# Kernel optimization log

Measured on AMD Instinct MI355X. Metric: run time of the kernel, lower is better.

Reference implementation:

```python
import jax, jax.numpy as jnp
import numpy as np

HEADS = 16
D_MODEL = 1024
D_K = D_MODEL // HEADS


def setup_inputs() -> dict:
    key = jax.random.key(0)
    ks = jax.random.split(key, 11)
    B, S = 4, 2048
    scale = 1.0 / np.sqrt(D_MODEL)
    inp = {
        "query": jax.random.normal(ks[0], (B, S, D_MODEL), dtype=jnp.float32),
        "key": jax.random.normal(ks[1], (B, S, D_MODEL), dtype=jnp.float32),
        "value": jax.random.normal(ks[2], (B, S, D_MODEL), dtype=jnp.float32),
        "Wq": jax.random.normal(ks[3], (D_MODEL, D_MODEL), dtype=jnp.float32) * scale,
        "bq": jnp.zeros((D_MODEL,), dtype=jnp.float32),
        "Wk": jax.random.normal(ks[4], (D_MODEL, D_MODEL), dtype=jnp.float32) * scale,
        "bk": jnp.zeros((D_MODEL,), dtype=jnp.float32),
        "Wv": jax.random.normal(ks[5], (D_MODEL, D_MODEL), dtype=jnp.float32) * scale,
        "bv": jnp.zeros((D_MODEL,), dtype=jnp.float32),
        "Wo": jax.random.normal(ks[6], (D_MODEL, D_MODEL), dtype=jnp.float32) * scale,
        "bo": jnp.zeros((D_MODEL,), dtype=jnp.float32),
    }
    return inp


def reference(query, key, value, Wq, bq, Wk, bk, Wv, bv, Wo, bo):
    B, S, _ = query.shape
    # Linear projections, split into heads: [B,S,D] -> [B,H,S,d_k]
    def proj(x, W, b):
        y = x @ W.T + b
        return y.reshape(B, S, HEADS, D_K).transpose(0, 2, 1, 3)

    q = proj(query, Wq, bq)
    k = proj(key, Wk, bk)
    v = proj(value, Wv, bv)

    scores = jnp.einsum("bhqd,bhkd->bhqk", q, k) / jnp.sqrt(jnp.float32(D_K))
    p_attn = jax.nn.softmax(scores, axis=-1)  # dropout is identity in eval
    x = jnp.einsum("bhqk,bhkd->bhqd", p_attn, v)
    x = x.transpose(0, 2, 1, 3).reshape(B, S, HEADS * D_K)
    return x @ Wo.T + bo
```

## Files before the change

kernel.cpp:

```cpp
#include <hip/hip_runtime.h>
#include <hip/hip_bf16.h>
#include <stdint.h>

#define D_MODEL 1024
#define HEADS   16
#define DK      64
#define BATCH   4
#define SEQ     2048
#define MROWS   (BATCH * SEQ)

typedef __attribute__((ext_vector_type(8))) short bf16x8;
typedef __attribute__((ext_vector_type(4))) float f32x4;
typedef __attribute__((ext_vector_type(4))) unsigned int u32x4;
typedef __attribute__((ext_vector_type(2))) unsigned int u32x2;

__device__ __forceinline__ unsigned pk2bf(float a, float b) {
  __hip_bfloat162 h = __float22bfloat162_rn(float2{a, b});
  union { __hip_bfloat162 h; unsigned u; } c; c.h = h;
  return c.u;
}
__device__ __forceinline__ unsigned short n2bf(float f) {
  __hip_bfloat16 h = __float2bfloat16(f);
  union { __hip_bfloat16 h; unsigned short s; } c; c.h = h;
  return c.s;
}

__device__ __forceinline__ void gl_lds16(const void* g, void* l) {
  __builtin_amdgcn_global_load_lds(
      (const __attribute__((address_space(1))) unsigned int*)g,
      (__attribute__((address_space(3))) unsigned int*)l, 16, 0, 0);
}

__device__ __forceinline__ int swz64(int row, int col) {
  return row * 64 + (col ^ ((row & 7) << 3));
}

__global__ __launch_bounds__(256) void cvt4(const float* __restrict__ w0, const float* __restrict__ w1,
                                            const float* __restrict__ w2, const float* __restrict__ w3,
                                            unsigned short* __restrict__ o0, unsigned short* __restrict__ o1,
                                            unsigned short* __restrict__ o2, unsigned short* __restrict__ o3) {
  const int which = blockIdx.x >> 10;
  const float* in; unsigned short* out;
  if (which == 0)      { in = w0; out = o0; }
  else if (which == 1) { in = w1; out = o1; }
  else if (which == 2) { in = w2; out = o2; }
  else                 { in = w3; out = o3; }
  const int i = ((blockIdx.x & 1023) * 256 + threadIdx.x) * 4;
  f32x4 v = *(const f32x4*)(in + i);
  u32x2 w;
  w[0] = pk2bf(v[0], v[1]);
  w[1] = pk2bf(v[2], v[3]);
  *(u32x2*)(out + i) = w;
}

__global__ __launch_bounds__(256) void qkv_gemm(const float* __restrict__ Aq, const float* __restrict__ Ak,
                                                const float* __restrict__ Av,
                                                const unsigned short* __restrict__ Bq,
                                                const unsigned short* __restrict__ Bk,
                                                const unsigned short* __restrict__ Bv,
                                                const float* __restrict__ bq_, const float* __restrict__ bk_,
                                                const float* __restrict__ bv_,
                                                unsigned short* __restrict__ Qo, unsigned short* __restrict__ Ko,
                                                unsigned short* __restrict__ Vo) {
  __shared__ unsigned short As[128 * 40];
  __shared__ unsigned short Bs[128 * 32];

  const int which = blockIdx.x >> 9;
  const int bx = blockIdx.x & 511;
  const float* Af = which == 0 ? Aq : which == 1 ? Ak : Av;
  const unsigned short* Bw = which == 0 ? Bq : which == 1 ? Bk : Bv;
  const float* bias = which == 0 ? bq_ : which == 1 ? bk_ : bv_;

  const int tid = threadIdx.x;
  const int lane = tid & 63, wid = tid >> 6;
  const int l16 = lane & 15, lg = lane >> 4;
  const int wrow = (wid >> 1) * 64, wcol = (wid & 1) * 64;

  const int swzb = (bx & 7) * 64 + (bx >> 3);
  const int m0 = (swzb >> 3) * 128, n0 = (swzb & 7) * 128;

  f32x4 acc[4][4];
  const f32x4 zero = {0.f, 0.f, 0.f, 0.f};
#pragma unroll
  for (int i = 0; i < 4; ++i)
#pragma unroll
    for (int j = 0; j < 4; ++j) acc[i][j] = zero;

#pragma unroll 1
  for (int kt = 0; kt < D_MODEL / 32; ++kt) {
    const int k0 = kt * 32;
    __syncthreads();
    {
      const int ar = tid >> 1, ah = (tid & 1) * 16;
      const float* src = Af + (size_t)(m0 + ar) * D_MODEL + k0 + ah;
      f32x4 v0 = *(const f32x4*)src;
      f32x4 v1 = *(const f32x4*)(src + 4);
      f32x4 v2 = *(const f32x4*)(src + 8);
      f32x4 v3 = *(const f32x4*)(src + 12);
      u32x4 pa, pb;
      pa[0] = pk2bf(v0[0], v0[1]);
      pa[1] = pk2bf(v0[2], v0[3]);
      pa[2] = pk2bf(v1[0], v1[1]);
      pa[3] = pk2bf(v1[2], v1[3]);
      pb[0] = pk2bf(v2[0], v2[1]);
      pb[1] = pk2bf(v2[2], v2[3]);
      pb[2] = pk2bf(v3[0], v3[1]);
      pb[3] = pk2bf(v3[2], v3[3]);
      *(u32x4*)&As[ar * 40 + ah] = pa;
      *(u32x4*)&As[ar * 40 + ah + 8] = pb;
    }
    {
      const unsigned short* srcb = Bw + (size_t)n0 * D_MODEL + k0;
#pragma unroll
      for (int p = 0; p < 2; ++p) {
        const int e = wid * 512 + p * 2048 + lane * 8;
        gl_lds16(srcb + (size_t)(e >> 5) * D_MODEL + (e & 31),
                 (char*)Bs + wid * 1024 + p * 4096);
      }
    }
    __syncthreads();

    bf16x8 af[4], bfr[4];
#pragma unroll
    for (int i = 0; i < 4; ++i) {
      af[i]  = *(const bf16x8*)&As[(wrow + i * 16 + l16) * 40 + lg * 8];
      bfr[i] = *(const bf16x8*)&Bs[(wcol + i * 16 + l16) * 32 + lg * 8];
    }
#pragma unroll
    for (int i = 0; i < 4; ++i)
#pragma unroll
      for (int j = 0; j < 4; ++j)
        acc[i][j] = __builtin_amdgcn_mfma_f32_16x16x32_bf16(af[i], bfr[j], acc[i][j], 0, 0, 0);
  }

#pragma unroll
  for (int j = 0; j < 4; ++j) {
    const int col = n0 + wcol + j * 16 + l16;
    const float bv = bias[col];
    if (which == 2) {
      const int hh = col >> 6, dd = col & 63;
#pragma unroll
      for (int i = 0; i < 4; ++i) {
        const int row0 = m0 + wrow + i * 16 + lg * 4;
        u32x2 pw;
        pw[0] = pk2bf(acc[i][j][0] + bv, acc[i][j][1] + bv);
        pw[1] = pk2bf(acc[i][j][2] + bv, acc[i][j][3] + bv);
        unsigned short* dst = Vo +
            ((((size_t)(row0 >> 11) * HEADS + hh) * DK + dd) * SEQ + (row0 & (SEQ - 1)));
        *(u32x2*)dst = pw;
      }
    } else {
      unsigned short* Outp = which == 0 ? Qo : Ko;
#pragma unroll
      for (int i = 0; i < 4; ++i) {
        const int row0 = m0 + wrow + i * 16 + lg * 4;
#pragma unroll
        for (int r = 0; r < 4; ++r)
          Outp[(size_t)(row0 + r) * D_MODEL + col] = n2bf(acc[i][j][r] + bv);
      }
    }
  }
}

__global__ __launch_bounds__(256) void out_gemm(const unsigned short* __restrict__ Ab,
                                                const unsigned short* __restrict__ Bw,
                                                const float* __restrict__ bias,
                                                float* __restrict__ Outp) {
  __shared__ unsigned short As[128 * 32];
  __shared__ unsigned short Bs[128 * 32];

  const int tid = threadIdx.x;
  const int lane = tid & 63, wid = tid >> 6;
  const int l16 = lane & 15, lg = lane >> 4;
  const int wrow = (wid >> 1) * 64, wcol = (wid & 1) * 64;

  const int bx = blockIdx.x;
  const int swzb = (bx & 7) * 64 + (bx >> 3);
  const int m0 = (swzb >> 3) * 128, n0 = (swzb & 7) * 128;

  f32x4 acc[4][4];
  const f32x4 zero = {0.f, 0.f, 0.f, 0.f};
#pragma unroll
  for (int i = 0; i < 4; ++i)
#pragma unroll
    for (int j = 0; j < 4; ++j) acc[i][j] = zero;

#pragma unroll 1
  for (int kt = 0; kt < D_MODEL / 32; ++kt) {
    const int k0 = kt * 32;
    __syncthreads();
    {
      const unsigned short* srcb = Ab + (size_t)m0 * D_MODEL + k0;
#pragma unroll
      for (int p = 0; p < 2; ++p) {
        const int e = wid * 512 + p * 2048 + lane * 8;
        gl_lds16(srcb + (size_t)(e >> 5) * D_MODEL + (e & 31),
                 (char*)As + wid * 1024 + p * 4096);
      }
    }
    {
      const unsigned short* srcb = Bw + (size_t)n0 * D_MODEL + k0;
#pragma unroll
      for (int p = 0; p < 2; ++p) {
        const int e = wid * 512 + p * 2048 + lane * 8;
        gl_lds16(srcb + (size_t)(e >> 5) * D_MODEL + (e & 31),
                 (char*)Bs + wid * 1024 + p * 4096);
      }
    }
    __syncthreads();

    bf16x8 af[4], bfr[4];
#pragma unroll
    for (int i = 0; i < 4; ++i) {
      af[i]  = *(const bf16x8*)&As[(wrow + i * 16 + l16) * 32 + lg * 8];
      bfr[i] = *(const bf16x8*)&Bs[(wcol + i * 16 + l16) * 32 + lg * 8];
    }
#pragma unroll
    for (int i = 0; i < 4; ++i)
#pragma unroll
      for (int j = 0; j < 4; ++j)
        acc[i][j] = __builtin_amdgcn_mfma_f32_16x16x32_bf16(af[i], bfr[j], acc[i][j], 0, 0, 0);
  }

#pragma unroll
  for (int j = 0; j < 4; ++j) {
    const int col = n0 + wcol + j * 16 + l16;
    const float bv = bias[col];
#pragma unroll
    for (int i = 0; i < 4; ++i) {
      const int row0 = m0 + wrow + i * 16 + lg * 4;
#pragma unroll
      for (int r = 0; r < 4; ++r)
        Outp[(size_t)(row0 + r) * D_MODEL + col] = acc[i][j][r] + bv;
    }
  }
}

__global__ __launch_bounds__(256, 2) void attn_v9(const unsigned short* __restrict__ Qb,
                                                  const unsigned short* __restrict__ Kb,
                                                  const unsigned short* __restrict__ Vtg,
                                                  unsigned short* __restrict__ Xo) {
  __shared__ unsigned short Ks[2][64 * 64];
  __shared__ unsigned short Vt[2][64 * 64];
  __shared__ unsigned short Ps[4][64 * 64];

  const int tid = threadIdx.x;
  const int lane = tid & 63, w = tid >> 6;
  const int l16 = lane & 15, lg = lane >> 4;

  const int p = blockIdx.x;
  const int lb = (p & 7) * 64 + (p >> 3);
  const int qb = lb & 7, bh = lb >> 3;
  const int b = bh >> 4, h = bh & 15;

  const size_t srow0 = (size_t)b * SEQ + qb * 256;
  const unsigned short* Qp = Qb + srow0 * D_MODEL + h * DK;
  const unsigned short* Kp = Kb + (size_t)b * SEQ * D_MODEL + h * DK;
  const unsigned short* Vp = Vtg + (size_t)bh * DK * SEQ;

  const int sr = tid >> 2;
  const int scol = (tid & 3) * 16;

  bf16x8 qfrag[4][2];
#pragma unroll
  for (int qf = 0; qf < 4; ++qf)
#pragma unroll
    for (int kh = 0; kh < 2; ++kh)
      qfrag[qf][kh] = *(const bf16x8*)(Qp + (size_t)(w * 64 + qf * 16 + l16) * D_MODEL + kh * 32 + lg * 8);

  u32x4 kr0, kr1, vr0, vr1;
  {
    const unsigned short* ksrc = Kp + (size_t)sr * D_MODEL + scol;
    kr0 = *(const u32x4*)ksrc; kr1 = *(const u32x4*)(ksrc + 8);
    const unsigned short* vsrc = Vp + (size_t)sr * SEQ + scol;
    vr0 = *(const u32x4*)vsrc; vr1 = *(const u32x4*)(vsrc + 8);
  }

  float lsum[4];
  f32x4 acco[4][4];
  const f32x4 zero = {0.f, 0.f, 0.f, 0.f};
#pragma unroll
  for (int qf = 0; qf < 4; ++qf) {
    lsum[qf] = 0.f;
#pragma unroll
    for (int df = 0; df < 4; ++df) acco[qf][df] = zero;
  }

  const float SC = 0.125f * 1.4426950408889634f;
  unsigned short* Psw = Ps[w];
  const int srcbase = (lane & 48) | ((lane & 48) >> 2);

#pragma unroll 1
  for (int kb = 0; kb < SEQ / 64; ++kb) {
    const int buf = kb & 1;
    *(u32x4*)&Ks[buf][swz64(sr, scol)] = kr0;
    *(u32x4*)&Ks[buf][swz64(sr, scol + 8)] = kr1;
    *(u32x4*)&Vt[buf][swz64(sr, scol)] = vr0;
    *(u32x4*)&Vt[buf][swz64(sr, scol + 8)] = vr1;
    __syncthreads();
    if (kb + 1 < SEQ / 64) {
      const unsigned short* ksrc = Kp + (size_t)((kb + 1) * 64 + sr) * D_MODEL + scol;
      kr0 = *(const u32x4*)ksrc; kr1 = *(const u32x4*)(ksrc + 8);
      const unsigned short* vsrc = Vp + (size_t)sr * SEQ + (kb + 1) * 64 + scol;
      vr0 = *(const u32x4*)vsrc; vr1 = *(const u32x4*)(vsrc + 8);
    }

    f32x4 sc[4][4];
#pragma unroll
    for (int qf = 0; qf < 4; ++qf)
#pragma unroll
      for (int tf = 0; tf < 4; ++tf) sc[qf][tf] = zero;
#pragma unroll
    for (int tf = 0; tf < 4; ++tf) {
      bf16x8 k0 = *(const bf16x8*)&Ks[buf][swz64(tf * 16 + l16, lg * 8)];
      bf16x8 k1 = *(const bf16x8*)&Ks[buf][swz64(tf * 16 + l16, 32 + lg * 8)];
#pragma unroll
      for (int qf = 0; qf < 4; ++qf) {
        sc[qf][tf] = __builtin_amdgcn_mfma_f32_16x16x32_bf16(k0, qfrag[qf][0], sc[qf][tf], 0, 0, 0);
        sc[qf][tf] = __builtin_amdgcn_mfma_f32_16x16x32_bf16(k1, qfrag[qf][1], sc[qf][tf], 0, 0, 0);
      }
    }

#pragma unroll
    for (int qf = 0; qf < 4; ++qf) {
      float sum = 0.f;
#pragma unroll
      for (int tf = 0; tf < 4; ++tf)
#pragma unroll
        for (int r = 0; r < 4; ++r) {
          const float pv = __builtin_amdgcn_exp2f(sc[qf][tf][r] * SC);
          sc[qf][tf][r] = pv;
          sum += pv;
        }
      lsum[qf] += sum;
#pragma unroll
      for (int tf = 0; tf < 4; ++tf) {
        u32x2 pw;
        pw[0] = pk2bf(sc[qf][tf][0], sc[qf][tf][1]);
        pw[1] = pk2bf(sc[qf][tf][2], sc[qf][tf][3]);
        *(u32x2*)&Psw[swz64(qf * 16 + l16, tf * 16 + lg * 4)] = pw;
      }
    }

    bf16x8 pf[4][2];
#pragma unroll
    for (int qf = 0; qf < 4; ++qf)
#pragma unroll
      for (int k2 = 0; k2 < 2; ++k2)
        pf[qf][k2] = *(const bf16x8*)&Psw[swz64(qf * 16 + l16, k2 * 32 + lg * 8)];

#pragma unroll
    for (int df = 0; df < 4; ++df) {
      bf16x8 v0 = *(const bf16x8*)&Vt[buf][swz64(df * 16 + l16, lg * 8)];
      bf16x8 v1 = *(const bf16x8*)&Vt[buf][swz64(df * 16 + l16, 32 + lg * 8)];
#pragma unroll
      for (int qf = 0; qf < 4; ++qf) {
        acco[qf][df] = __builtin_amdgcn_mfma_f32_16x16x32_bf16(pf[qf][0], v0, acco[qf][df], 0, 0, 0);
        acco[qf][df] = __builtin_amdgcn_mfma_f32_16x16x32_bf16(pf[qf][1], v1, acco[qf][df], 0, 0, 0);
      }
    }
  }

#pragma unroll
  for (int qf = 0; qf < 4; ++qf) {
    lsum[qf] += __shfl_xor(lsum[qf], 16);
    lsum[qf] += __shfl_xor(lsum[qf], 32);
  }

  unsigned short* dst = Xo + (srow0 + w * 64) * D_MODEL + h * DK;
#pragma unroll
  for (int qf = 0; qf < 4; ++qf) {
    const float inv = 1.f / lsum[qf];
#pragma unroll
    for (int r = 0; r < 4; ++r) {
      const float rr = __shfl(inv, srcbase + r);
      const int row = qf * 16 + lg * 4 + r;
#pragma unroll
      for (int df = 0; df < 4; ++df)
        dst[(size_t)row * D_MODEL + df * 16 + l16] = n2bf(acco[qf][df][r] * rr);
    }
  }
}

extern "C" void kernel_launch(void* const* d_in, const int* in_sizes, int n_in,
                              void* d_out, int out_size, void* d_ws, size_t ws_size,
                              hipStream_t stream) {
  const float* query = (const float*)d_in[0];
  const float* key_  = (const float*)d_in[1];
  const float* value = (const float*)d_in[2];
  const float* Wq = (const float*)d_in[3];
  const float* bq = (const float*)d_in[4];
  const float* Wk = (const float*)d_in[5];
  const float* bk = (const float*)d_in[6];
  const float* Wv = (const float*)d_in[7];
  const float* bv = (const float*)d_in[8];
  const float* Wo = (const float*)d_in[9];
  const float* bo = (const float*)d_in[10];

  unsigned short* ws  = (unsigned short*)d_ws;
  unsigned short* WqB = ws;
  unsigned short* WkB = WqB + (1u << 20);
  unsigned short* WvB = WkB + (1u << 20);
  unsigned short* WoB = WvB + (1u << 20);
  unsigned short* Qb  = WoB + (1u << 20);
  unsigned short* Kb  = Qb + (size_t)MROWS * D_MODEL;
  unsigned short* Vtg = Kb + (size_t)MROWS * D_MODEL;
  unsigned short* Xb  = Vtg + (size_t)MROWS * D_MODEL;
  if (ws_size < (size_t)(4u * (1u << 20) + 4u * (size_t)MROWS * D_MODEL) * 2u) return;

  cvt4<<<4096, 256, 0, stream>>>(Wq, Wk, Wv, Wo, WqB, WkB, WvB, WoB);

  qkv_gemm<<<1536, 256, 0, stream>>>(query, key_, value, WqB, WkB, WvB, bq, bk, bv, Qb, Kb, Vtg);

  attn_v9<<<512, 256, 0, stream>>>(Qb, Kb, Vtg, Xb);

  out_gemm<<<512, 256, 0, stream>>>(Xb, WoB, bo, (float*)d_out);
}
```

Before: 241.0 us.

## Double-buffer GEMM LDS tiles with register prefetch and fold softmax scale into Q

Both projection GEMMs switch from a single LDS buffer filled by direct global-to-LDS loads to two LDS buffers filled from registers. The next K-tile is loaded into registers while the current tile is consumed, so each iteration needs one barrier instead of two and global latency is hidden behind MFMA work. Separately, the softmax scale (1/sqrt(dk)·log2e) is applied to Q in the QKV epilogue, which removes one multiply per score in the attention kernel. The cost is more LDS and register pressure, and the scaled Q is rounded to bf16 after scaling, which changes rounding slightly.

```diff
diff --git a/kernel.cpp b/kernel.cpp
--- a/kernel.cpp
+++ b/kernel.cpp
@@ -14,6 +14,8 @@
 typedef __attribute__((ext_vector_type(4))) unsigned int u32x4;
 typedef __attribute__((ext_vector_type(2))) unsigned int u32x2;
 
+#define SCQ 0.18033688011112042f
+
 __device__ __forceinline__ unsigned pk2bf(float a, float b) {
   __hip_bfloat162 h = __float22bfloat162_rn(float2{a, b});
   union { __hip_bfloat162 h; unsigned u; } c; c.h = h;
@@ -23,12 +25,6 @@
   __hip_bfloat16 h = __float2bfloat16(f);
   union { __hip_bfloat16 h; unsigned short s; } c; c.h = h;
   return c.s;
-}
-
-__device__ __forceinline__ void gl_lds16(const void* g, void* l) {
-  __builtin_amdgcn_global_load_lds(
-      (const __attribute__((address_space(1))) unsigned int*)g,
-      (__attribute__((address_space(3))) unsigned int*)l, 16, 0, 0);
 }
 
 __device__ __forceinline__ int swz64(int row, int col) {
@@ -62,8 +58,8 @@
                                                 const float* __restrict__ bv_,
                                                 unsigned short* __restrict__ Qo, unsigned short* __restrict__ Ko,
                                                 unsigned short* __restrict__ Vo) {
-  __shared__ unsigned short As[128 * 40];
-  __shared__ unsigned short Bs[128 * 32];
+  __shared__ unsigned short As[2][128 * 40];
+  __shared__ unsigned short Bs[2][128 * 32];
 
   const int which = blockIdx.x >> 9;
   const int bx = blockIdx.x & 511;
@@ -79,6 +75,10 @@
   const int swzb = (bx & 7) * 64 + (bx >> 3);
   const int m0 = (swzb >> 3) * 128, n0 = (swzb & 7) * 128;
 
+  const int sr2 = tid >> 1, sc16 = (tid & 1) * 16;
+  const float* aSrc = Af + (size_t)(m0 + sr2) * D_MODEL + sc16;
+  const unsigned short* bSrc = Bw + (size_t)(n0 + sr2) * D_MODEL + sc16;
+
   f32x4 acc[4][4];
   const f32x4 zero = {0.f, 0.f, 0.f, 0.f};
 #pragma unroll
@@ -86,45 +86,36 @@
 #pragma unroll
     for (int j = 0; j < 4; ++j) acc[i][j] = zero;
 
+  f32x4 a0 = *(const f32x4*)aSrc, a1 = *(const f32x4*)(aSrc + 4),
+        a2 = *(const f32x4*)(aSrc + 8), a3 = *(const f32x4*)(aSrc + 12);
+  u32x4 br0 = *(const u32x4*)bSrc, br1 = *(const u32x4*)(bSrc + 8);
+
 #pragma unroll 1
   for (int kt = 0; kt < D_MODEL / 32; ++kt) {
-    const int k0 = kt * 32;
+    const int buf = kt & 1;
+    u32x4 pa, pb;
+    pa[0] = pk2bf(a0[0], a0[1]); pa[1] = pk2bf(a0[2], a0[3]);
+    pa[2] = pk2bf(a1[0], a1[1]); pa[3] = pk2bf(a1[2], a1[3]);
+    pb[0] = pk2bf(a2[0], a2[1]); pb[1] = pk2bf(a2[2], a2[3]);
+    pb[2] = pk2bf(a3[0], a3[1]); pb[3] = pk2bf(a3[2], a3[3]);
+    *(u32x4*)&As[buf][sr2 * 40 + sc16] = pa;
+    *(u32x4*)&As[buf][sr2 * 40 + sc16 + 8] = pb;
+    *(u32x4*)&Bs[buf][sr2 * 32 + sc16] = br0;
+    *(u32x4*)&Bs[buf][sr2 * 32 + sc16 + 8] = br1;
     __syncthreads();
-    {
-      const int ar = tid >> 1, ah = (tid & 1) * 16;
-      const float* src = Af + (size_t)(m0 + ar) * D_MODEL + k0 + ah;
-      f32x4 v0 = *(const f32x4*)src;
-      f32x4 v1 = *(const f32x4*)(src + 4);
-      f32x4 v2 = *(const f32x4*)(src + 8);
-      f32x4 v3 = *(const f32x4*)(src + 12);
-      u32x4 pa, pb;
-      pa[0] = pk2bf(v0[0], v0[1]);
-      pa[1] = pk2bf(v0[2], v0[3]);
-      pa[2] = pk2bf(v1[0], v1[1]);
-      pa[3] = pk2bf(v1[2], v1[3]);
-      pb[0] = pk2bf(v2[0], v2[1]);
-      pb[1] = pk2bf(v2[2], v2[3]);
-      pb[2] = pk2bf(v3[0], v3[1]);
-      pb[3] = pk2bf(v3[2], v3[3]);
-      *(u32x4*)&As[ar * 40 + ah] = pa;
-      *(u32x4*)&As[ar * 40 + ah + 8] = pb;
-    }
-    {
-      const unsigned short* srcb = Bw + (size_t)n0 * D_MODEL + k0;
-#pragma unroll
-      for (int p = 0; p < 2; ++p) {
-        const int e = wid * 512 + p * 2048 + lane * 8;
-        gl_lds16(srcb + (size_t)(e >> 5) * D_MODEL + (e & 31),
-                 (char*)Bs + wid * 1024 + p * 4096);
-      }
-    }
-    __syncthreads();
+    if (kt + 1 < D_MODEL / 32) {
+      const float* an = aSrc + (kt + 1) * 32;
+      a0 = *(const f32x4*)an; a1 = *(const f32x4*)(an + 4);
+      a2 = *(const f32x4*)(an + 8); a3 = *(const f32x4*)(an + 12);
+      const unsigned short* bn = bSrc + (kt + 1) * 32;
+      br0 = *(const u32x4*)bn; br1 = *(const u32x4*)(bn + 8);
+    }
 
     bf16x8 af[4], bfr[4];
 #pragma unroll
     for (int i = 0; i < 4; ++i) {
-      af[i]  = *(const bf16x8*)&As[(wrow + i * 16 + l16) * 40 + lg * 8];
-      bfr[i] = *(const bf16x8*)&Bs[(wcol + i * 16 + l16) * 32 + lg * 8];
+      af[i]  = *(const bf16x8*)&As[buf][(wrow + i * 16 + l16) * 40 + lg * 8];
+      bfr[i] = *(const bf16x8*)&Bs[buf][(wcol + i * 16 + l16) * 32 + lg * 8];
     }
 #pragma unroll
     for (int i = 0; i < 4; ++i)
@@ -133,6 +124,7 @@
         acc[i][j] = __builtin_amdgcn_mfma_f32_16x16x32_bf16(af[i], bfr[j], acc[i][j], 0, 0, 0);
   }
 
+  const float scale = (which == 0) ? SCQ : 1.0f;
 #pragma unroll
   for (int j = 0; j < 4; ++j) {
     const int col = n0 + wcol + j * 16 + l16;
@@ -156,7 +148,7 @@
         const int row0 = m0 + wrow + i * 16 + lg * 4;
 #pragma unroll
         for (int r = 0; r < 4; ++r)
-          Outp[(size_t)(row0 + r) * D_MODEL + col] = n2bf(acc[i][j][r] + bv);
+          Outp[(size_t)(row0 + r) * D_MODEL + col] = n2bf((acc[i][j][r] + bv) * scale);
       }
     }
   }
@@ -166,8 +158,8 @@
                                                 const unsigned short* __restrict__ Bw,
                                                 const float* __restrict__ bias,
                                                 float* __restrict__ Outp) {
-  __shared__ unsigned short As[128 * 32];
-  __shared__ unsigned short Bs[128 * 32];
+  __shared__ unsigned short As[2][128 * 32];
+  __shared__ unsigned short Bs[2][128 * 32];
 
   const int tid = threadIdx.x;
   const int lane = tid & 63, wid = tid >> 6;
@@ -178,6 +170,10 @@
   const int swzb = (bx & 7) * 64 + (bx >> 3);
   const int m0 = (swzb >> 3) * 128, n0 = (swzb & 7) * 128;
 
+  const int sr2 = tid >> 1, sc16 = (tid & 1) * 16;
+  const unsigned short* aSrc = Ab + (size_t)(m0 + sr2) * D_MODEL + sc16;
+  const unsigned short* bSrc = Bw + (size_t)(n0 + sr2) * D_MODEL + sc16;
+
   f32x4 acc[4][4];
   const f32x4 zero = {0.f, 0.f, 0.f, 0.f};
 #pragma unroll
@@ -185,35 +181,29 @@
 #pragma unroll
     for (int j = 0; j < 4; ++j) acc[i][j] = zero;
 
+  u32x4 ar0 = *(const u32x4*)aSrc, ar1 = *(const u32x4*)(aSrc + 8);
+  u32x4 br0 = *(const u32x4*)bSrc, br1 = *(const u32x4*)(bSrc + 8);
+
 #pragma unroll 1
   for (int kt = 0; kt < D_MODEL / 32; ++kt) {
-    const int k0 = kt * 32;
+    const int buf = kt & 1;
+    *(u32x4*)&As[buf][sr2 * 32 + sc16] = ar0;
+    *(u32x4*)&As[buf][sr2 * 32 + sc16 + 8] = ar1;
+    *(u32x4*)&Bs[buf][sr2 * 32 + sc16] = br0;
+    *(u32x4*)&Bs[buf][sr2 * 32 + sc16 + 8] = br1;
     __syncthreads();
-    {
-      const unsigned short* srcb = Ab + (size_t)m0 * D_MODEL + k0;
-#pragma unroll
-      for (int p = 0; p < 2; ++p) {
-        const int e = wid * 512 + p * 2048 + lane * 8;
-        gl_lds16(srcb + (size_t)(e >> 5) * D_MODEL + (e & 31),
-                 (char*)As + wid * 1024 + p * 4096);
-      }
-    }
-    {
-      const unsigned short* srcb = Bw + (size_t)n0 * D_MODEL + k0;
-#pragma unroll
-      for (int p = 0; p < 2; ++p) {
-        const int e = wid * 512 + p * 2048 + lane * 8;
-        gl_lds16(srcb + (size_t)(e >> 5) * D_MODEL + (e & 31),
-                 (char*)Bs + wid * 1024 + p * 4096);
-      }
-    }
-    __syncthreads();
+    if (kt + 1 < D_MODEL / 32) {
+      const unsigned short* an = aSrc + (kt + 1) * 32;
+      ar0 = *(const u32x4*)an; ar1 = *(const u32x4*)(an + 8);
+      const unsigned short* bn = bSrc + (kt + 1) * 32;
+      br0 = *(const u32x4*)bn; br1 = *(const u32x4*)(bn + 8);
+    }
 
     bf16x8 af[4], bfr[4];
 #pragma unroll
     for (int i = 0; i < 4; ++i) {
-      af[i]  = *(const bf16x8*)&As[(wrow + i * 16 + l16) * 32 + lg * 8];
-      bfr[i] = *(const bf16x8*)&Bs[(wcol + i * 16 + l16) * 32 + lg * 8];
+      af[i]  = *(const bf16x8*)&As[buf][(wrow + i * 16 + l16) * 32 + lg * 8];
+      bfr[i] = *(const bf16x8*)&Bs[buf][(wcol + i * 16 + l16) * 32 + lg * 8];
     }
 #pragma unroll
     for (int i = 0; i < 4; ++i)
@@ -236,10 +226,10 @@
   }
 }
 
-__global__ __launch_bounds__(256, 2) void attn_v9(const unsigned short* __restrict__ Qb,
-                                                  const unsigned short* __restrict__ Kb,
-                                                  const unsigned short* __restrict__ Vtg,
-                                                  unsigned short* __restrict__ Xo) {
+__global__ __launch_bounds__(256, 2) void attn_v10(const unsigned short* __restrict__ Qb,
+                                                   const unsigned short* __restrict__ Kb,
+                                                   const unsigned short* __restrict__ Vtg,
+                                                   unsigned short* __restrict__ Xo) {
   __shared__ unsigned short Ks[2][64 * 64];
   __shared__ unsigned short Vt[2][64 * 64];
   __shared__ unsigned short Ps[4][64 * 64];
@@ -286,7 +276,6 @@
     for (int df = 0; df < 4; ++df) acco[qf][df] = zero;
   }
 
-  const float SC = 0.125f * 1.4426950408889634f;
   unsigned short* Psw = Ps[w];
   const int srcbase = (lane & 48) | ((lane & 48) >> 2);
 
@@ -328,7 +317,7 @@
       for (int tf = 0; tf < 4; ++tf)
 #pragma unroll
         for (int r = 0; r < 4; ++r) {
-          const float pv = __builtin_amdgcn_exp2f(sc[qf][tf][r] * SC);
+          const float pv = __builtin_amdgcn_exp2f(sc[qf][tf][r]);
           sc[qf][tf][r] = pv;
           sum += pv;
         }
@@ -412,7 +401,7 @@
 
   qkv_gemm<<<1536, 256, 0, stream>>>(query, key_, value, WqB, WkB, WvB, bq, bk, bv, Qb, Kb, Vtg);
 
-  attn_v9<<<512, 256, 0, stream>>>(Qb, Kb, Vtg, Xb);
+  attn_v10<<<512, 256, 0, stream>>>(Qb, Kb, Vtg, Xb);
 
   out_gemm<<<512, 256, 0, stream>>>(Xb, WoB, bo, (float*)d_out);
 }
```

Result: faster. 208.7 us (-13.4%).
